# Kernel tuning notes

Measured on AMD Instinct MI355X. Metric: run time of the kernel, lower is better.

Reference implementation:

```python
import jax, jax.numpy as jnp
import numpy as np

K = 3       # conv-transpose kernel size
STRIDE = 2  # conv-transpose stride
PAD = 1     # conv-transpose padding
POOL = 6    # fused pool: MaxPool3d(2,2) then MaxPool3d(3,3) == MaxPool3d(6,6)


def setup_inputs() -> dict:
    key = jax.random.key(0)
    k1, k2, k3 = jax.random.split(key, 3)
    x = jax.random.normal(k1, (8, 16, 32, 32, 32), dtype=jnp.float32)
    weight = jax.random.normal(k2, (16, 32, K, K, K), dtype=jnp.float32)  # [C_in, C_out, k, k, k]
    bias = jax.random.normal(k3, (32,), dtype=jnp.float32)
    return {"x": x, "weight": weight, "bias": bias}


def _conv_transpose3d(x, weight, bias):
    # Transposed conv as dilated conv: lhs_dilation=stride, pad k-1-p, flip kernel.
    # weight layout [C_in, C_out, kd, kh, kw] matches kernel spec 'IODHW'.
    pad = K - 1 - PAD
    y = jax.lax.conv_general_dilated(
        x,
        jnp.flip(weight, axis=(2, 3, 4)),
        window_strides=(1, 1, 1),
        padding=[(pad, pad)] * 3,
        lhs_dilation=(STRIDE, STRIDE, STRIDE),
        dimension_numbers=("NCDHW", "IODHW", "NCDHW"),
    )
    return y + bias[None, :, None, None, None]


def reference(x, weight, bias):
    y = _conv_transpose3d(x, weight, bias)  # [N, C_out, 63, 63, 63]
    n, c, d, h, w = y.shape
    do, ho, wo = d // POOL, h // POOL, w // POOL
    # fused non-overlapping 6x6x6 max pool (== MaxPool3d(2) -> MaxPool3d(3))
    y = y[:, :, : do * POOL, : ho * POOL, : wo * POOL]
    y = y.reshape(n, c, do, POOL, ho, POOL, wo, POOL).max(axis=(3, 5, 7))
    # channel sum, keepdim -> [N, 1, do, ho, wo]
    return jnp.sum(y, axis=1, keepdims=True)
```

## Files before the change

kernel.cpp:

```cpp
#include <hip/hip_runtime.h>
#include <hip/hip_bf16.h>
#include <math.h>


namespace {

typedef __attribute__((ext_vector_type(8))) short short8;
typedef __attribute__((ext_vector_type(16))) float f32x16;

__device__ __forceinline__ uint f2bf(float f) {
  uint u = __float_as_uint(f);
  return (u + 0x7FFFu + ((u >> 16) & 1u)) >> 16;
}

__global__ void prep_w(const float* __restrict__ w, ushort* __restrict__ w2) {
  const int o = blockIdx.x * 256 + threadIdx.x;
  const int j = o >> 9;
  const int cih = (o >> 8) & 1;
  const int co = (o >> 3) & 31;
  const int ci = cih * 8 + (o & 7);
  w2[o] = (ushort)f2bf(w[(ci * 32 + co) * 27 + j]);
}

template <int PA, int PB, int PC>
__device__ __forceinline__ float cls_max(const short8 (&bq)[27],
                                         const char* __restrict__ xw, int lin0,
                                         int lin1, int sz0, int sz1, int hi) {
  f32x16 d;
#pragma unroll
  for (int i = 0; i < 16; ++i) d[i] = 0.f;
#pragma unroll
  for (int a = 0; a < (PA ? 2 : 1); ++a) {
    const int kd = PA ? (a ? 2 : 0) : 1;
    const int oz = PA ? (a ? 0 : 1) : 0;
#pragma unroll
    for (int b = 0; b < (PB ? 2 : 1); ++b) {
      const int kh = PB ? (b ? 2 : 0) : 1;
      const int oy = PB ? (b ? 0 : 1) : 0;
#pragma unroll
      for (int c = 0; c < (PC ? 2 : 1); ++c) {
        const int kw = PC ? (c ? 2 : 0) : 1;
        const int ox = PC ? (c ? 0 : 1) : 0;
        const int addr =
            ((oz ? lin1 : lin0) + (oy * 4 + ox) * 48) ^ (oz ? sz1 : sz0);
        const short8 av = *reinterpret_cast<const short8*>(xw + addr);
        d = __builtin_amdgcn_mfma_f32_32x32x16_bf16(av, bq[kd * 9 + kh * 3 + kw],
                                                    d, 0, 0, 0);
      }
    }
  }
  float ma = d[0];
#pragma unroll
  for (int i = 1; i < 12; ++i) ma = fmaxf(ma, d[i]);
  const float mb = fmaxf(d[12], fmaxf(d[13], d[14]));
  float vm = hi ? ma : fmaxf(ma, mb);
  vm = fmaxf(vm, __shfl_xor(vm, 32));
  return vm;
}

__global__ __launch_bounds__(256, 2) void fused_mfma(
    const float* __restrict__ x, const ushort* __restrict__ w2,
    const float* __restrict__ bias, float* __restrict__ out) {
  __shared__ __align__(16) char xls[4 * 3072];

  const int t = threadIdx.x;
  const int wv = t >> 6;
  const int l = t & 63;
  const int hi = l >> 5;
  const int co = l & 31;

  const int cell = blockIdx.x * 4 + wv;
  const int pw = cell % 10;
  const int ph = (cell / 10) % 10;
  const int pd = (cell / 100) % 10;
  const int n = cell / 1000;

  short8 bq[27];
#pragma unroll
  for (int tp = 0; tp < 27; ++tp)
    bq[tp] = *reinterpret_cast<const short8*>(w2 + tp * 512 + hi * 256 + co * 8);

  char* xw = xls + wv * 3072;
  {
    const int xi = l & 3, yi = (l >> 2) & 3, zi = l >> 4;
    const float* xg = x + (size_t)n * 524288 + (size_t)(3 * pd + zi) * 1024 +
                      (3 * ph + yi) * 32 + (3 * pw + xi);
    uint pk[8];
#pragma unroll
    for (int q = 0; q < 8; ++q) {
      const uint h0 = f2bf(xg[(2 * q) * 32768]);
      const uint h1 = f2bf(xg[(2 * q + 1) * 32768]);
      pk[q] = (h0 & 0xFFFFu) | (h1 << 16);
    }
    const int swz = (zi & 3) << 4;
    const int a0 = (l * 48) ^ swz;
    const int a1 = (l * 48 + 16) ^ swz;
    *reinterpret_cast<uint4*>(xw + a0) = make_uint4(pk[0], pk[1], pk[2], pk[3]);
    *reinterpret_cast<uint4*>(xw + a1) = make_uint4(pk[4], pk[5], pk[6], pk[7]);
  }
  asm volatile("s_waitcnt lgkmcnt(0)" ::: "memory");

  int p = co > 26 ? 26 : co;
  const int ip = p / 9, jp = (p / 3) % 3, kp = p % 3;
  const int lin0 = (ip * 16 + jp * 4 + kp) * 48 + hi * 16;
  const int lin1 = ((ip + 1) * 16 + jp * 4 + kp) * 48 + hi * 16;
  const int sz0 = (ip & 3) << 4;
  const int sz1 = ((ip + 1) & 3) << 4;

  float cm = cls_max<0, 0, 0>(bq, xw, lin0, lin1, sz0, sz1, hi);
  cm = fmaxf(cm, cls_max<0, 0, 1>(bq, xw, lin0, lin1, sz0, sz1, hi));
  cm = fmaxf(cm, cls_max<0, 1, 0>(bq, xw, lin0, lin1, sz0, sz1, hi));
  cm = fmaxf(cm, cls_max<0, 1, 1>(bq, xw, lin0, lin1, sz0, sz1, hi));
  cm = fmaxf(cm, cls_max<1, 0, 0>(bq, xw, lin0, lin1, sz0, sz1, hi));
  cm = fmaxf(cm, cls_max<1, 0, 1>(bq, xw, lin0, lin1, sz0, sz1, hi));
  cm = fmaxf(cm, cls_max<1, 1, 0>(bq, xw, lin0, lin1, sz0, sz1, hi));
  cm = fmaxf(cm, cls_max<1, 1, 1>(bq, xw, lin0, lin1, sz0, sz1, hi));

  float r = cm + bias[co];
#pragma unroll
  for (int off = 16; off >= 1; off >>= 1) r += __shfl_xor(r, off);
  if (l == 0) out[cell] = r;
}

}

extern "C" void kernel_launch(void* const* d_in, const int* in_sizes, int n_in,
                              void* d_out, int out_size, void* d_ws,
                              size_t ws_size, hipStream_t stream) {
  const float* x = (const float*)d_in[0];
  const float* w = (const float*)d_in[1];
  const float* b = (const float*)d_in[2];
  float* out = (float*)d_out;
  ushort* w2 = (ushort*)d_ws;
  prep_w<<<54, 256, 0, stream>>>(w, w2);
  fused_mfma<<<2000, 256, 0, stream>>>(x, w2, b, out);
}
```

Baseline: 82.30 us.

## Stream weights per parity class instead of holding all taps in registers

Removes the 27-entry register array of weight fragments. Weights are repacked so each parity class's taps are contiguous and are loaded from global memory (L2-resident) just before use. Launch bounds are raised to 4 blocks per SIMD-equivalent to exploit the lower VGPR pressure, and the cross-half shuffle is hoisted out of the per-class reduction into a single final shuffle. The trade-off is repeated global/L2 weight loads inside the compute sequence, which could stall MFMAs if latency is not hidden.

```diff
diff --git a/kernel.cpp b/kernel.cpp
--- a/kernel.cpp
+++ b/kernel.cpp
@@ -8,6 +8,9 @@
 typedef __attribute__((ext_vector_type(8))) short short8;
 typedef __attribute__((ext_vector_type(16))) float f32x16;
 
+__constant__ int JK[27] = {13, 12, 14, 10, 16, 9,  11, 15, 17, 4,  22, 3,  5, 21,
+                           23, 1,  7,  19, 25, 0,  2,  6,  8,  18, 20, 24, 26};
+
 __device__ __forceinline__ uint f2bf(float f) {
   uint u = __float_as_uint(f);
   return (u + 0x7FFFu + ((u >> 16) & 1u)) >> 16;
@@ -15,37 +18,41 @@
 
 __global__ void prep_w(const float* __restrict__ w, ushort* __restrict__ w2) {
   const int o = blockIdx.x * 256 + threadIdx.x;
-  const int j = o >> 9;
+  const int t2 = o >> 9;
   const int cih = (o >> 8) & 1;
   const int co = (o >> 3) & 31;
   const int ci = cih * 8 + (o & 7);
-  w2[o] = (ushort)f2bf(w[(ci * 32 + co) * 27 + j]);
+  w2[o] = (ushort)f2bf(w[(ci * 32 + co) * 27 + JK[t2]]);
 }
 
-template <int PA, int PB, int PC>
-__device__ __forceinline__ float cls_max(const short8 (&bq)[27],
+template <int PA, int PB, int PC, int BASE>
+__device__ __forceinline__ float cls_max(const ushort* __restrict__ w2l,
                                          const char* __restrict__ xw, int lin0,
                                          int lin1, int sz0, int sz1, int hi) {
+  constexpr int NTZ = PA ? 2 : 1, NTY = PB ? 2 : 1, NTX = PC ? 2 : 1;
+  constexpr int NT = NTZ * NTY * NTX;
+  short8 bv[NT];
+#pragma unroll
+  for (int t = 0; t < NT; ++t)
+    bv[t] = *reinterpret_cast<const short8*>(w2l + (BASE + t) * 512);
+
   f32x16 d;
 #pragma unroll
   for (int i = 0; i < 16; ++i) d[i] = 0.f;
 #pragma unroll
-  for (int a = 0; a < (PA ? 2 : 1); ++a) {
-    const int kd = PA ? (a ? 2 : 0) : 1;
+  for (int a = 0; a < NTZ; ++a) {
     const int oz = PA ? (a ? 0 : 1) : 0;
 #pragma unroll
-    for (int b = 0; b < (PB ? 2 : 1); ++b) {
-      const int kh = PB ? (b ? 2 : 0) : 1;
+    for (int b = 0; b < NTY; ++b) {
       const int oy = PB ? (b ? 0 : 1) : 0;
 #pragma unroll
-      for (int c = 0; c < (PC ? 2 : 1); ++c) {
-        const int kw = PC ? (c ? 2 : 0) : 1;
+      for (int c = 0; c < NTX; ++c) {
         const int ox = PC ? (c ? 0 : 1) : 0;
         const int addr =
             ((oz ? lin1 : lin0) + (oy * 4 + ox) * 48) ^ (oz ? sz1 : sz0);
         const short8 av = *reinterpret_cast<const short8*>(xw + addr);
-        d = __builtin_amdgcn_mfma_f32_32x32x16_bf16(av, bq[kd * 9 + kh * 3 + kw],
-                                                    d, 0, 0, 0);
+        d = __builtin_amdgcn_mfma_f32_32x32x16_bf16(
+            av, bv[(a * NTY + b) * NTX + c], d, 0, 0, 0);
       }
     }
   }
@@ -53,12 +60,10 @@
 #pragma unroll
   for (int i = 1; i < 12; ++i) ma = fmaxf(ma, d[i]);
   const float mb = fmaxf(d[12], fmaxf(d[13], d[14]));
-  float vm = hi ? ma : fmaxf(ma, mb);
-  vm = fmaxf(vm, __shfl_xor(vm, 32));
-  return vm;
+  return hi ? ma : fmaxf(ma, mb);
 }
 
-__global__ __launch_bounds__(256, 2) void fused_mfma(
+__global__ __launch_bounds__(256, 4) void fused_mfma(
     const float* __restrict__ x, const ushort* __restrict__ w2,
     const float* __restrict__ bias, float* __restrict__ out) {
   __shared__ __align__(16) char xls[4 * 3072];
@@ -74,11 +79,6 @@
   const int ph = (cell / 10) % 10;
   const int pd = (cell / 100) % 10;
   const int n = cell / 1000;
-
-  short8 bq[27];
-#pragma unroll
-  for (int tp = 0; tp < 27; ++tp)
-    bq[tp] = *reinterpret_cast<const short8*>(w2 + tp * 512 + hi * 256 + co * 8);
 
   char* xw = xls + wv * 3072;
   {
@@ -107,14 +107,17 @@
   const int sz0 = (ip & 3) << 4;
   const int sz1 = ((ip + 1) & 3) << 4;
 
-  float cm = cls_max<0, 0, 0>(bq, xw, lin0, lin1, sz0, sz1, hi);
-  cm = fmaxf(cm, cls_max<0, 0, 1>(bq, xw, lin0, lin1, sz0, sz1, hi));
-  cm = fmaxf(cm, cls_max<0, 1, 0>(bq, xw, lin0, lin1, sz0, sz1, hi));
-  cm = fmaxf(cm, cls_max<0, 1, 1>(bq, xw, lin0, lin1, sz0, sz1, hi));
-  cm = fmaxf(cm, cls_max<1, 0, 0>(bq, xw, lin0, lin1, sz0, sz1, hi));
-  cm = fmaxf(cm, cls_max<1, 0, 1>(bq, xw, lin0, lin1, sz0, sz1, hi));
-  cm = fmaxf(cm, cls_max<1, 1, 0>(bq, xw, lin0, lin1, sz0, sz1, hi));
-  cm = fmaxf(cm, cls_max<1, 1, 1>(bq, xw, lin0, lin1, sz0, sz1, hi));
+  const ushort* w2l = w2 + hi * 256 + co * 8;
+
+  float cm = cls_max<1, 1, 1, 19>(w2l, xw, lin0, lin1, sz0, sz1, hi);
+  cm = fmaxf(cm, cls_max<1, 1, 0, 15>(w2l, xw, lin0, lin1, sz0, sz1, hi));
+  cm = fmaxf(cm, cls_max<1, 0, 1, 11>(w2l, xw, lin0, lin1, sz0, sz1, hi));
+  cm = fmaxf(cm, cls_max<1, 0, 0, 9>(w2l, xw, lin0, lin1, sz0, sz1, hi));
+  cm = fmaxf(cm, cls_max<0, 1, 1, 5>(w2l, xw, lin0, lin1, sz0, sz1, hi));
+  cm = fmaxf(cm, cls_max<0, 1, 0, 3>(w2l, xw, lin0, lin1, sz0, sz1, hi));
+  cm = fmaxf(cm, cls_max<0, 0, 1, 1>(w2l, xw, lin0, lin1, sz0, sz1, hi));
+  cm = fmaxf(cm, cls_max<0, 0, 0, 0>(w2l, xw, lin0, lin1, sz0, sz1, hi));
+  cm = fmaxf(cm, __shfl_xor(cm, 32));
 
   float r = cm + bias[co];
 #pragma unroll
```

Result: no change. 81.96 us (-0.4%).
